# Kernel optimization log

Measured on AMD Instinct MI355X. Metric: run time of the kernel, lower is better.

## Reference

```python
import jax, jax.numpy as jnp
import numpy as np

Vx, Vy, B, N, C, H, M_VIEWS = 8, 8, 4, 196, 768, 12, 4
DH = C // H
SCALE = DH ** -0.5
HID = 4 * C


def _layer_norm(x, w, b, eps=1e-5):
    mu = jnp.mean(x, axis=-1, keepdims=True)
    var = jnp.mean((x - mu) ** 2, axis=-1, keepdims=True)
    return (x - mu) / jnp.sqrt(var + eps) * w + b


def setup_inputs() -> dict:
    key = jax.random.key(0)
    ks = jax.random.split(key, 32)
    s = 0.02
    inp = {
        "xs": jax.random.normal(ks[0], (Vx, B, N, C), jnp.float32),
        "ys": jax.random.normal(ks[1], (Vy, B, N, C), jnp.float32),
        "xposes": jax.random.randint(ks[2], (Vx, B, N, 2), 0, N),
        "yposes": jax.random.randint(ks[3], (Vy, B, N, 2), 0, N),
        "rel_ids": jax.random.randint(ks[4], (Vx * M_VIEWS,), 0, Vy),
        "M": M_VIEWS,
        # self-attention params (qkv_bias=False, proj has bias)
        "qkv_w": jax.random.normal(ks[5], (3 * C, C), jnp.float32) * s,
        "attn_proj_w": jax.random.normal(ks[6], (C, C), jnp.float32) * s,
        "attn_proj_b": jnp.zeros((C,), jnp.float32),
        # cross-attention params
        "q_w": jax.random.normal(ks[7], (C, C), jnp.float32) * s,
        "k_w": jax.random.normal(ks[8], (C, C), jnp.float32) * s,
        "v_w": jax.random.normal(ks[9], (C, C), jnp.float32) * s,
        "cross_proj_w": jax.random.normal(ks[10], (C, C), jnp.float32) * s,
        "cross_proj_b": jnp.zeros((C,), jnp.float32),
        # MLP
        "fc1_w": jax.random.normal(ks[11], (HID, C), jnp.float32) * s,
        "fc1_b": jnp.zeros((HID,), jnp.float32),
        "fc2_w": jax.random.normal(ks[12], (C, HID), jnp.float32) * s,
        "fc2_b": jnp.zeros((C,), jnp.float32),
        # layer norms
        "ln1_w": jnp.ones((C,), jnp.float32), "ln1_b": jnp.zeros((C,), jnp.float32),
        "ln2_w": jnp.ones((C,), jnp.float32), "ln2_b": jnp.zeros((C,), jnp.float32),
        "ln3_w": jnp.ones((C,), jnp.float32), "ln3_b": jnp.zeros((C,), jnp.float32),
        "lny_w": jnp.ones((C,), jnp.float32), "lny_b": jnp.zeros((C,), jnp.float32),
    }
    return inp


def _forward(xs, ys, rel_ids, M,
             qkv_w, attn_proj_w, attn_proj_b,
             q_w, k_w, v_w, cross_proj_w, cross_proj_b,
             fc1_w, fc1_b, fc2_w, fc2_b,
             ln1_w, ln1_b, ln2_w, ln2_b, ln3_w, ln3_b, lny_w, lny_b):
    vx, b, nx, c = xs.shape
    vy, _, ny, _ = ys.shape
    x = xs.reshape(vx * b, nx, c)

    # ---- self-attention over each target view (rope=None) ----
    h = _layer_norm(x, ln1_w, ln1_b)
    qkv = (h @ qkv_w.T).reshape(vx * b, nx, 3, H, DH)
    q = jnp.transpose(qkv[:, :, 0], (0, 2, 1, 3))  # (VB,H,N,dh)
    k = jnp.transpose(qkv[:, :, 1], (0, 2, 1, 3))
    v = jnp.transpose(qkv[:, :, 2], (0, 2, 1, 3))
    attn = jax.nn.softmax(jnp.einsum('bhnd,bhkd->bhnk', q, k) * SCALE, axis=-1)
    o = jnp.einsum('bhnk,bhkd->bnhd', attn, v).reshape(vx * b, nx, c)
    x = x + (o @ attn_proj_w.T + attn_proj_b)

    # ---- batched multi-view cross-attention ----
    xn = _layer_norm(x.reshape(vx, b, nx, c), ln2_w, ln2_b)
    yn = _layer_norm(ys, lny_w, lny_b)
    qs = (xn @ q_w.T).reshape(vx, b, nx, H, DH)
    ks = (yn @ k_w.T).reshape(vy, b, ny, H, DH)
    vs = (yn @ v_w.T).reshape(vy, b, ny, H, DH)
    ks_r = ks[rel_ids].reshape(vx, M, b, ny, H, DH)  # index_select + group
    vs_r = vs[rel_ids].reshape(vx, M, b, ny, H, DH)
    # q is broadcast across the M group dim (no materialized expand)
    scores = jnp.einsum('vbnhd,vmbkhd->vmbhnk', qs, ks_r) * SCALE
    a = jax.nn.softmax(scores, axis=-1)
    o = jnp.einsum('vmbhnk,vmbkhd->vmbnhd', a, vs_r).reshape(vx, M, b, nx, c)
    o = o @ cross_proj_w.T + cross_proj_b  # (Vx,M,B,Nx,C)
    merged = jnp.max(o, axis=1).reshape(vx * b, nx, c)  # max-merge over M
    x = x + merged

    # ---- MLP ----
    h = _layer_norm(x, ln3_w, ln3_b)
    x = x + (jax.nn.gelu(h @ fc1_w.T + fc1_b, approximate=False) @ fc2_w.T + fc2_b)
    return x.reshape(vx, b, nx, c)


def reference(xs, ys, xposes, yposes, rel_ids, M,
              qkv_w, attn_proj_w, attn_proj_b,
              q_w, k_w, v_w, cross_proj_w, cross_proj_b,
              fc1_w, fc1_b, fc2_w, fc2_b,
              ln1_w, ln1_b, ln2_w, ln2_b, ln3_w, ln3_b, lny_w, lny_b):
    # xposes/yposes unused because rope=None in this configuration
    return _forward(xs, ys, rel_ids, M,
                    qkv_w, attn_proj_w, attn_proj_b,
                    q_w, k_w, v_w, cross_proj_w, cross_proj_b,
                    fc1_w, fc1_b, fc2_w, fc2_b,
                    ln1_w, ln1_b, ln2_w, ln2_b, ln3_w, ln3_b, lny_w, lny_b)
```

## Files before the change

kernel.cpp:

```cpp
#include <hip/hip_runtime.h>
#include <hip/hip_bf16.h>
#include <stdint.h>
#include <math.h>

#define H_ 12
#define NQ 196
#define CD 768
#define HIDD 3072
#define VX 8
#define VY 8
#define BB 4
#define MV 4
#define VBB 32
#define ROWS 6272
#define CROSS_ROWS 25088
#define SCALE_LOG2E 0.180336880260608f

typedef __attribute__((ext_vector_type(8))) short short8;
typedef __attribute__((ext_vector_type(4))) float f32x4;
typedef __attribute__((ext_vector_type(4))) unsigned short u16x4;
typedef unsigned short u16;

#define AS1 __attribute__((address_space(1)))
#define AS3 __attribute__((address_space(3)))

__device__ __forceinline__ float bf2f(u16 u){
  union { unsigned int i; float f; } v; v.i = ((unsigned int)u) << 16; return v.f;
}
__device__ __forceinline__ u16 f2bf(float f){
  union { unsigned int i; float f; } v; v.f = f;
  return (u16)((v.i + 0x7fff + ((v.i >> 16) & 1)) >> 16);
}
__device__ __forceinline__ unsigned int f2u(float f){
  union { unsigned int i; float f; } v; v.f = f; return v.i;
}

struct CastSegs {
  const float* src[8];
  u16* dst[8];
  int cum[9];
};
__global__ __launch_bounds__(256) void k_cast_all(CastSegs segs){
  int i = blockIdx.x * 256 + threadIdx.x;
  if (i >= segs.cum[8]) return;
  int s = 0;
  #pragma unroll
  for (int k = 1; k < 8; k++) s += (i >= segs.cum[k]);
  const int off = i - segs.cum[s];
  segs.dst[s][off] = f2bf(segs.src[s][off]);
}

__device__ __forceinline__ void ln_row(const float* __restrict__ x,
    const float* __restrict__ w, const float* __restrict__ b,
    u16* __restrict__ out, int row, int tid){
  const float* xr = x + (size_t)row * CD;
  float v0 = xr[tid], v1 = xr[tid + 256], v2 = xr[tid + 512];
  float s  = v0 + v1 + v2;
  float s2 = v0*v0 + v1*v1 + v2*v2;
  __shared__ float red[8];
  const int lane = tid & 63, wid = tid >> 6;
  #pragma unroll
  for (int o = 32; o; o >>= 1){ s += __shfl_down(s, o); s2 += __shfl_down(s2, o); }
  if (lane == 0){ red[wid] = s; red[wid + 4] = s2; }
  __syncthreads();
  if (tid == 0){
    red[0] = red[0] + red[1] + red[2] + red[3];
    red[4] = red[4] + red[5] + red[6] + red[7];
  }
  __syncthreads();
  const float mu   = red[0] * (1.f/768.f);
  const float var  = red[4] * (1.f/768.f) - mu*mu;
  const float rstd = rsqrtf(var + 1e-5f);
  u16* orow = out + (size_t)row * CD;
  orow[tid]       = f2bf((v0 - mu)*rstd*w[tid]       + b[tid]);
  orow[tid + 256] = f2bf((v1 - mu)*rstd*w[tid + 256] + b[tid + 256]);
  orow[tid + 512] = f2bf((v2 - mu)*rstd*w[tid + 512] + b[tid + 512]);
}

__global__ __launch_bounds__(256) void k_ln_bf16(const float* __restrict__ x,
    const float* __restrict__ w, const float* __restrict__ b, u16* __restrict__ out){
  ln_row(x, w, b, out, blockIdx.x, threadIdx.x);
}

__global__ __launch_bounds__(256) void k_ln_bf16x2(
    const float* __restrict__ x0, const float* __restrict__ w0,
    const float* __restrict__ b0, u16* __restrict__ o0,
    const float* __restrict__ x1, const float* __restrict__ w1,
    const float* __restrict__ b1, u16* __restrict__ o1){
  const int bid = blockIdx.x;
  if (bid < ROWS) ln_row(x0, w0, b0, o0, bid, threadIdx.x);
  else            ln_row(x1, w1, b1, o1, bid - ROWS, threadIdx.x);
}

__global__ __launch_bounds__(256) void k_mmln(const u16* __restrict__ op,
    float* __restrict__ x, const float* __restrict__ w, const float* __restrict__ b,
    u16* __restrict__ out){
  const int row = blockIdx.x, tid = threadIdx.x;
  const int n = row % NQ, vb = row / NQ;
  const int vx = vb >> 2, bb = vb & 3;
  const size_t r0 = ((size_t)(vx * MV) * BB + bb) * NQ + n;
  const size_t ms = (size_t)BB * NQ;
  float* xr = x + (size_t)row * CD;
  float v[3], s = 0.f, s2 = 0.f;
  #pragma unroll
  for (int j = 0; j < 3; j++){
    const int col = tid + j*256;
    float mx =        bf2f(op[(r0       ) * CD + col]);
    mx = fmaxf(mx,    bf2f(op[(r0 +   ms) * CD + col]));
    mx = fmaxf(mx,    bf2f(op[(r0 + 2*ms) * CD + col]));
    mx = fmaxf(mx,    bf2f(op[(r0 + 3*ms) * CD + col]));
    const float val = xr[col] + mx;
    xr[col] = val;
    v[j] = val;
    s += val; s2 += val*val;
  }
  __shared__ float red[8];
  const int lane = tid & 63, wid = tid >> 6;
  #pragma unroll
  for (int o = 32; o; o >>= 1){ s += __shfl_down(s, o); s2 += __shfl_down(s2, o); }
  if (lane == 0){ red[wid] = s; red[wid + 4] = s2; }
  __syncthreads();
  if (tid == 0){
    red[0] = red[0] + red[1] + red[2] + red[3];
    red[4] = red[4] + red[5] + red[6] + red[7];
  }
  __syncthreads();
  const float mu   = red[0] * (1.f/768.f);
  const float var  = red[4] * (1.f/768.f) - mu*mu;
  const float rstd = rsqrtf(var + 1e-5f);
  u16* orow = out + (size_t)row * CD;
  #pragma unroll
  for (int j = 0; j < 3; j++){
    const int col = tid + j*256;
    orow[col] = f2bf((v[j] - mu)*rstd*w[col] + b[col]);
  }
}

template<int EPI, int TM, int DB>
__global__ __launch_bounds__(256) void k_gemm_bt(
    const u16* __restrict__ A, const u16* __restrict__ B,
    float* __restrict__ Cf, u16* __restrict__ Cb,
    const float* __restrict__ bias, const float* __restrict__ resid,
    int M, int N, int K){
  __shared__ u16 As[(DB + 1) * TM * 64];
  __shared__ u16 Bs[(DB + 1) * 128 * 64];
  const int tid  = threadIdx.x;
  const int lane = tid & 63;
  const int wave = tid >> 6;
  const int wr = wave >> 1, wc = wave & 1;

  const int gx = gridDim.x;
  const int nwg = gx * gridDim.y;
  const int orig = blockIdx.y * gx + blockIdx.x;
  const int q8 = nwg >> 3, r8 = nwg & 7;
  const int xcd = orig & 7, bse = orig >> 3;
  const int wg = (xcd < r8 ? xcd * (q8 + 1) : r8 * (q8 + 1) + (xcd - r8) * q8) + bse;
  const int m0 = (wg / gx) * TM, n0 = (wg % gx) * 128;

  f32x4 acc[TM/32][4];
  #pragma unroll
  for (int i = 0; i < TM/32; i++)
    #pragma unroll
    for (int j = 0; j < 4; j++) acc[i][j] = (f32x4){0.f, 0.f, 0.f, 0.f};

  const int lrow = lane >> 3;
  const int lcol = ((lane & 7) ^ lrow) * 8;
  const u16* arow = A + (size_t)(m0 + wave*(TM/4) + lrow) * K + lcol;
  const u16* brow = B + (size_t)(n0 + wave*32 + lrow) * K + lcol;

  auto STG = [&](int nb, int k0){
    #pragma unroll
    for (int i = 0; i < TM/32; i++)
      __builtin_amdgcn_global_load_lds(
        (const AS1 void*)(arow + (size_t)i*8*K + k0),
        (AS3 void*)(As + nb*TM*64 + (wave*(TM/4) + i*8)*64), 16, 0, 0);
    #pragma unroll
    for (int i = 0; i < 4; i++)
      __builtin_amdgcn_global_load_lds(
        (const AS1 void*)(brow + (size_t)i*8*K + k0),
        (AS3 void*)(Bs + nb*128*64 + (wave*32 + i*8)*64), 16, 0, 0);
  };

  auto COMPUTE = [&](int nb){
    const u16* ab = As + nb*TM*64 + (wr*(TM/2) + (lane & 15))*64;
    const u16* bb = Bs + nb*128*64 + (wc*64 + (lane & 15))*64;
    const int r7 = lane & 7;
    #pragma unroll
    for (int kk = 0; kk < 2; kk++){
      const int sl = (((lane >> 4) + 4*kk) ^ r7) * 8;
      short8 af[TM/32], bfr[4];
      #pragma unroll
      for (int f = 0; f < TM/32; f++) af[f] = *(const short8*)(ab + f*1024 + sl);
      #pragma unroll
      for (int f = 0; f < 4; f++)     bfr[f] = *(const short8*)(bb + f*1024 + sl);
      #pragma unroll
      for (int i = 0; i < TM/32; i++)
        #pragma unroll
        for (int j = 0; j < 4; j++)
          acc[i][j] = __builtin_amdgcn_mfma_f32_16x16x32_bf16(af[i], bfr[j], acc[i][j], 0, 0, 0);
    }
  };

  if (DB){
    const int NT = K >> 6;
    STG(0, 0);
    __syncthreads();
    for (int it = 0; it < NT; ++it){
      const int cb = it & 1;
      if (it + 1 < NT) STG(cb ^ 1, (it + 1) * 64);
      COMPUTE(cb);
      __syncthreads();
    }
  } else {
    for (int k0 = 0; k0 < K; k0 += 64){
      STG(0, k0);
      __syncthreads();
      COMPUTE(0);
      __syncthreads();
    }
  }

  #pragma unroll
  for (int i = 0; i < TM/32; i++){
    const int rb = m0 + wr*(TM/2) + i*16 + (lane >> 4)*4;
    #pragma unroll
    for (int j = 0; j < 4; j++){
      const int col = n0 + wc*64 + j*16 + (lane & 15);
      #pragma unroll
      for (int r = 0; r < 4; r++){
        const size_t idx = (size_t)(rb + r) * N + col;
        const float v = acc[i][j][r];
        if (EPI == 0){
          Cb[idx] = f2bf(v);
        } else if (EPI == 1){
          Cf[idx] = v + bias[col] + resid[idx];
        } else if (EPI == 2){
          Cf[idx] = v + bias[col];
        } else if (EPI == 3){
          float g = v + bias[col];
          g = 0.5f * g * (1.f + erff(g * 0.70710678118654752f));
          Cb[idx] = f2bf(g);
        } else {
          Cb[idx] = f2bf(v + bias[col]);
        }
      }
    }
  }
}

template<int MODE>
__global__ __launch_bounds__(256) void k_attn_mfma(
    const u16* __restrict__ Qb, const u16* __restrict__ Kb, const u16* __restrict__ Vb,
    u16* __restrict__ Ob, const int* __restrict__ rel_ids){
  __shared__ u16 Kl[2][2048];
  __shared__ u16 Vl[2][2048];

  size_t qbase, kbase, vbase, obase;
  int qstr, kstr;
  if (MODE == 0){
    const int vb = blockIdx.x / H_, h = blockIdx.x % H_;
    qbase = (size_t)vb * NQ * 2304 + h * 64; qstr = 2304;
    kbase = qbase + 768; vbase = qbase + 1536; kstr = 2304;
    obase = (size_t)vb * NQ * CD + h * 64;
  } else {
    const int h = blockIdx.x % H_; int t = blockIdx.x / H_;
    const int b = t % BB; t /= BB;
    const int m = t % MV; const int vx = t / MV;
    const int rel = rel_ids[vx * MV + m];
    qbase = ((size_t)(vx * BB + b) * NQ) * CD + h * 64; qstr = CD;
    kbase = ((size_t)(rel * BB + b) * NQ) * 1536 + h * 64; kstr = 1536;
    vbase = kbase + 768;
    obase = ((size_t)((vx * MV + m) * BB + b) * NQ) * CD + h * 64;
  }

  const int tid  = threadIdx.x;
  const int lane = tid & 63;
  const int wave = tid >> 6;
  const int lq   = lane & 15;
  const int g    = lane >> 4;

  short8 qfrag[4][2];
  #pragma unroll
  for (int qf = 0; qf < 4; qf++){
    int qrow = wave*64 + qf*16 + lq; if (qrow > 195) qrow = 195;
    const u16* qp = Qb + qbase + (size_t)qrow * qstr + g*8;
    qfrag[qf][0] = *(const short8*)(qp);
    qfrag[qf][1] = *(const short8*)(qp + 32);
  }

  f32x4 oacc[4][4];
  #pragma unroll
  for (int i = 0; i < 4; i++)
    #pragma unroll
    for (int j = 0; j < 4; j++) oacc[i][j] = (f32x4){0.f,0.f,0.f,0.f};
  float l_[4] = {0.f, 0.f, 0.f, 0.f};

  const int skey  = tid >> 3;
  const int sslot = (tid & 7) ^ (skey & 7);
  const int vkey = lane >> 1;
  const int vdh  = wave*16 + (lane & 1)*8;

  auto STAGE = [&](int nb, int t0n){
    int kg = t0n + skey; if (kg > 195) kg = 195;
    __builtin_amdgcn_global_load_lds(
        (const AS1 void*)(Kb + kbase + (size_t)kg*kstr + sslot*8),
        (AS3 void*)(&Kl[nb][wave*512]), 16, 0, 0);
    int vg = t0n + vkey; if (vg > 195) vg = 195;
    __builtin_amdgcn_global_load_lds(
        (const AS1 void*)(Vb + vbase + (size_t)vg*kstr + vdh),
        (AS3 void*)(&Vl[nb][wave*512]), 16, 0, 0);
  };

  union U8 { unsigned u[4]; short8 s; };

  STAGE(0, 0);
  __syncthreads();

  for (int t = 0; t < 7; t++){
    const int cb = t & 1;
    const int t0 = t * 32;
    if (t < 6) STAGE(cb ^ 1, t0 + 32);

    f32x4 sacc[4][2];
    #pragma unroll
    for (int qf = 0; qf < 4; qf++)
      #pragma unroll
      for (int kf = 0; kf < 2; kf++) sacc[qf][kf] = (f32x4){0.f,0.f,0.f,0.f};
    __builtin_amdgcn_s_setprio(1);
    #pragma unroll
    for (int kf = 0; kf < 2; kf++){
      const int key = kf*16 + lq;
      #pragma unroll
      for (int ks = 0; ks < 2; ks++){
        short8 kfrag = *(const short8*)(&Kl[cb][key*64 + (((ks<<2) + g) ^ (key & 7))*8]);
        #pragma unroll
        for (int qf = 0; qf < 4; qf++)
          if (wave*64 + qf*16 < NQ)
            sacc[qf][kf] = __builtin_amdgcn_mfma_f32_16x16x32_bf16(kfrag, qfrag[qf][ks], sacc[qf][kf], 0, 0, 0);
      }
    }
    __builtin_amdgcn_s_setprio(0);

    const AS3 u16* vp = (const AS3 u16*)(&Vl[cb][0]) + (size_t)lane*4;
    uint2 tr0a, tr0b, tr1a, tr1b, tr2a, tr2b, tr3a, tr3b;
    asm volatile("ds_read_b64_tr_b16 %0, %1 offset:0"    : "=&v"(tr0a) : "v"(vp));
    asm volatile("ds_read_b64_tr_b16 %0, %1 offset:512"  : "=&v"(tr0b) : "v"(vp));
    asm volatile("ds_read_b64_tr_b16 %0, %1 offset:1024" : "=&v"(tr1a) : "v"(vp));
    asm volatile("ds_read_b64_tr_b16 %0, %1 offset:1536" : "=&v"(tr1b) : "v"(vp));
    asm volatile("ds_read_b64_tr_b16 %0, %1 offset:2048" : "=&v"(tr2a) : "v"(vp));
    asm volatile("ds_read_b64_tr_b16 %0, %1 offset:2560" : "=&v"(tr2b) : "v"(vp));
    asm volatile("ds_read_b64_tr_b16 %0, %1 offset:3072" : "=&v"(tr3a) : "v"(vp));
    asm volatile("ds_read_b64_tr_b16 %0, %1 offset:3584" : "=&v"(tr3b) : "v"(vp));

    short8 vfrag[4];
    #pragma unroll
    for (int qf = 0; qf < 4; qf++){
      if (wave*64 + qf*16 >= NQ) continue;
      float p[8], ps = 0.f;
      #pragma unroll
      for (int kf = 0; kf < 2; kf++)
        #pragma unroll
        for (int r = 0; r < 4; r++){
          const int key = t0 + kf*16 + g*4 + r;
          const float e = exp2f(sacc[qf][kf][r] * SCALE_LOG2E);
          p[kf*4 + r] = (key < 196) ? e : 0.f;
          ps += p[kf*4 + r];
        }
      ps += __shfl_xor(ps, 16);
      ps += __shfl_xor(ps, 32);
      l_[qf] += ps;
      U8 pk;
      pk.u[0] = (f2u(p[0]) >> 16) | (f2u(p[1]) & 0xffff0000u);
      pk.u[1] = (f2u(p[2]) >> 16) | (f2u(p[3]) & 0xffff0000u);
      pk.u[2] = (f2u(p[4]) >> 16) | (f2u(p[5]) & 0xffff0000u);
      pk.u[3] = (f2u(p[6]) >> 16) | (f2u(p[7]) & 0xffff0000u);

      if (qf == 0){
        asm volatile("s_waitcnt lgkmcnt(0)" ::: "memory");
        __builtin_amdgcn_sched_barrier(0);
        U8 v0; v0.u[0]=tr0a.x; v0.u[1]=tr0a.y; v0.u[2]=tr0b.x; v0.u[3]=tr0b.y; vfrag[0]=v0.s;
        U8 v1; v1.u[0]=tr1a.x; v1.u[1]=tr1a.y; v1.u[2]=tr1b.x; v1.u[3]=tr1b.y; vfrag[1]=v1.s;
        U8 v2; v2.u[0]=tr2a.x; v2.u[1]=tr2a.y; v2.u[2]=tr2b.x; v2.u[3]=tr2b.y; vfrag[2]=v2.s;
        U8 v3; v3.u[0]=tr3a.x; v3.u[1]=tr3a.y; v3.u[2]=tr3b.x; v3.u[3]=tr3b.y; vfrag[3]=v3.s;
      }
      __builtin_amdgcn_s_setprio(1);
      #pragma unroll
      for (int dhf = 0; dhf < 4; dhf++)
        oacc[qf][dhf] = __builtin_amdgcn_mfma_f32_16x16x32_bf16(vfrag[dhf], pk.s, oacc[qf][dhf], 0, 0, 0);
      __builtin_amdgcn_s_setprio(0);
    }
    __syncthreads();
  }

  #pragma unroll
  for (int qf = 0; qf < 4; qf++){
    const int qrow = wave*64 + qf*16 + lq;
    if (qrow < 196){
      const float inv = 1.f / l_[qf];
      u16* orow = Ob + obase + (size_t)qrow * CD;
      #pragma unroll
      for (int dhf = 0; dhf < 4; dhf++){
        uint2 pk;
        pk.x = (unsigned)f2bf(oacc[qf][dhf][0]*inv) | ((unsigned)f2bf(oacc[qf][dhf][1]*inv) << 16);
        pk.y = (unsigned)f2bf(oacc[qf][dhf][2]*inv) | ((unsigned)f2bf(oacc[qf][dhf][3]*inv) << 16);
        *(uint2*)(orow + dhf*16 + g*4) = pk;
      }
    }
  }
}

extern "C" void kernel_launch(void* const* d_in, const int* in_sizes, int n_in,
                              void* d_out, int out_size, void* d_ws, size_t ws_size,
                              hipStream_t stream){
  const float* xs           = (const float*)d_in[0];
  const float* ys           = (const float*)d_in[1];
  const int*   rel_ids      = (const int*)  d_in[4];
  const float* qkv_w        = (const float*)d_in[6];
  const float* attn_proj_w  = (const float*)d_in[7];
  const float* attn_proj_b  = (const float*)d_in[8];
  const float* q_w          = (const float*)d_in[9];
  const float* k_w          = (const float*)d_in[10];
  const float* v_w          = (const float*)d_in[11];
  const float* cross_proj_w = (const float*)d_in[12];
  const float* cross_proj_b = (const float*)d_in[13];
  const float* fc1_w        = (const float*)d_in[14];
  const float* fc1_b        = (const float*)d_in[15];
  const float* fc2_w        = (const float*)d_in[16];
  const float* fc2_b        = (const float*)d_in[17];
  const float* ln1_w        = (const float*)d_in[18];
  const float* ln1_b        = (const float*)d_in[19];
  const float* ln2_w        = (const float*)d_in[20];
  const float* ln2_b        = (const float*)d_in[21];
  const float* ln3_w        = (const float*)d_in[22];
  const float* ln3_b        = (const float*)d_in[23];
  const float* lny_w        = (const float*)d_in[24];
  const float* lny_b        = (const float*)d_in[25];
  float* out = (float*)d_out;

  char* ws = (char*)d_ws;
  size_t off = 0;
  auto alloc = [&](size_t bytes) -> char* {
    char* p = ws + off; off += (bytes + 255) & ~(size_t)255; return p;
  };
  u16* wb_qkv   = (u16*)alloc((size_t)2304*768*2);
  u16* wb_aproj = (u16*)alloc((size_t)768*768*2);
  u16* wb_q     = (u16*)alloc((size_t)768*768*2);
  u16* wb_kv    = (u16*)alloc((size_t)1536*768*2);
  u16* wb_cproj = (u16*)alloc((size_t)768*768*2);
  u16* wb_fc1   = (u16*)alloc((size_t)3072*768*2);
  u16* wb_fc2   = (u16*)alloc((size_t)768*3072*2);
  float* x_ws   = (float*)alloc((size_t)ROWS*CD*4);
  u16* hbuf     = (u16*)alloc((size_t)ROWS*CD*2);
  u16* ynbuf    = (u16*)alloc((size_t)ROWS*CD*2);
  u16* o_self   = (u16*)alloc((size_t)ROWS*CD*2);
  u16* qs       = (u16*)alloc((size_t)ROWS*CD*2);
  u16* kvs      = (u16*)alloc((size_t)ROWS*1536*2);
  u16* o_cross  = (u16*)alloc((size_t)CROSS_ROWS*CD*2);
  char* un = alloc((size_t)CROSS_ROWS*CD*2);
  u16* qkvbuf = (u16*)un;
  u16* oproj  = (u16*)un;
  u16* mid    = (u16*)un;

  CastSegs segs;
  const float* srcs[8] = {qkv_w, attn_proj_w, q_w, k_w, v_w, cross_proj_w, fc1_w, fc2_w};
  u16* dsts[8] = {wb_qkv, wb_aproj, wb_q, wb_kv, wb_kv + 768*768, wb_cproj, wb_fc1, wb_fc2};
  int lens[8]  = {2304*768, 768*768, 768*768, 768*768, 768*768, 768*768, 3072*768, 3072*768};
  segs.cum[0] = 0;
  for (int i = 0; i < 8; i++){ segs.src[i] = srcs[i]; segs.dst[i] = dsts[i];
                               segs.cum[i+1] = segs.cum[i] + lens[i]; }
  k_cast_all<<<(segs.cum[8] + 255) / 256, 256, 0, stream>>>(segs);

  k_ln_bf16<<<ROWS, 256, 0, stream>>>(xs, ln1_w, ln1_b, hbuf);
  k_gemm_bt<0,128,0><<<dim3(2304/128, ROWS/128), 256, 0, stream>>>(
      hbuf, wb_qkv, nullptr, qkvbuf, nullptr, nullptr, ROWS, 2304, 768);
  k_attn_mfma<0><<<VBB * H_, 256, 0, stream>>>(qkvbuf, qkvbuf, qkvbuf, o_self, rel_ids);
  k_gemm_bt<1,64,1><<<dim3(768/128, ROWS/64), 256, 0, stream>>>(
      o_self, wb_aproj, x_ws, nullptr, attn_proj_b, xs, ROWS, 768, 768);

  k_ln_bf16x2<<<2*ROWS, 256, 0, stream>>>(x_ws, ln2_w, ln2_b, hbuf,
                                          ys, lny_w, lny_b, ynbuf);
  k_gemm_bt<0,64,1><<<dim3(768/128, ROWS/64), 256, 0, stream>>>(
      hbuf, wb_q, nullptr, qs, nullptr, nullptr, ROWS, 768, 768);
  k_gemm_bt<0,128,0><<<dim3(1536/128, ROWS/128), 256, 0, stream>>>(
      ynbuf, wb_kv, nullptr, kvs, nullptr, nullptr, ROWS, 1536, 768);
  k_attn_mfma<1><<<VX * MV * BB * H_, 256, 0, stream>>>(qs, kvs, kvs, o_cross, rel_ids);
  k_gemm_bt<4,128,0><<<dim3(768/128, CROSS_ROWS/128), 256, 0, stream>>>(
      o_cross, wb_cproj, nullptr, oproj, cross_proj_b, nullptr, CROSS_ROWS, 768, 768);
  k_mmln<<<ROWS, 256, 0, stream>>>(oproj, x_ws, ln3_w, ln3_b, hbuf);

  k_gemm_bt<3,128,0><<<dim3(HIDD/128, ROWS/128), 256, 0, stream>>>(
      hbuf, wb_fc1, nullptr, mid, fc1_b, nullptr, ROWS, HIDD, 768);
  k_gemm_bt<1,64,1><<<dim3(768/128, ROWS/64), 256, 0, stream>>>(
      mid, wb_fc2, out, nullptr, fc2_b, x_ws, ROWS, 768, HIDD);
}
```

Measured before the change: 380.9 us.

## Fold softmax scale into Q GEMM epilogue and compute row sums via MFMA

Adds a GEMM epilogue that multiplies the Q columns by scale*log2e before the bf16 store, so attention exponentiates raw scores without a per-element multiply. The softmax denominator is now accumulated with an extra MFMA against a vector of bf16 ones, which replaces the per-element sums and cross-lane shuffles. Key-boundary masking runs only on the last tile, and the row-validity guards around the MFMAs are dropped so the unrolled loops are uniform. In exchange, Q is rounded to bf16 after scaling, the denominator is summed from bf16-rounded probabilities, and padded query rows do redundant MFMA work.

```diff
diff --git a/kernel.cpp b/kernel.cpp
--- a/kernel.cpp
+++ b/kernel.cpp
@@ -240,8 +240,10 @@
           float g = v + bias[col];
           g = 0.5f * g * (1.f + erff(g * 0.70710678118654752f));
           Cb[idx] = f2bf(g);
+        } else if (EPI == 4){
+          Cb[idx] = f2bf(v + bias[col]);
         } else {
-          Cb[idx] = f2bf(v + bias[col]);
+          Cb[idx] = f2bf(col < 768 ? v * SCALE_LOG2E : v);
         }
       }
     }
@@ -288,12 +290,19 @@
     qfrag[qf][1] = *(const short8*)(qp + 32);
   }
 
+  union U8 { unsigned u[4]; short8 s; };
+
   f32x4 oacc[4][4];
   #pragma unroll
   for (int i = 0; i < 4; i++)
     #pragma unroll
     for (int j = 0; j < 4; j++) oacc[i][j] = (f32x4){0.f,0.f,0.f,0.f};
-  float l_[4] = {0.f, 0.f, 0.f, 0.f};
+  f32x4 lacc[4];
+  #pragma unroll
+  for (int i = 0; i < 4; i++) lacc[i] = (f32x4){0.f,0.f,0.f,0.f};
+  U8 ones;
+  #pragma unroll
+  for (int i = 0; i < 4; i++) ones.u[i] = 0x3F803F80u;
 
   const int skey  = tid >> 3;
   const int sslot = (tid & 7) ^ (skey & 7);
@@ -311,8 +320,6 @@
         (AS3 void*)(&Vl[nb][wave*512]), 16, 0, 0);
   };
 
-  union U8 { unsigned u[4]; short8 s; };
-
   STAGE(0, 0);
   __syncthreads();
 
@@ -335,8 +342,7 @@
         short8 kfrag = *(const short8*)(&Kl[cb][key*64 + (((ks<<2) + g) ^ (key & 7))*8]);
         #pragma unroll
         for (int qf = 0; qf < 4; qf++)
-          if (wave*64 + qf*16 < NQ)
-            sacc[qf][kf] = __builtin_amdgcn_mfma_f32_16x16x32_bf16(kfrag, qfrag[qf][ks], sacc[qf][kf], 0, 0, 0);
+          sacc[qf][kf] = __builtin_amdgcn_mfma_f32_16x16x32_bf16(kfrag, qfrag[qf][ks], sacc[qf][kf], 0, 0, 0);
       }
     }
     __builtin_amdgcn_s_setprio(0);
@@ -355,20 +361,19 @@
     short8 vfrag[4];
     #pragma unroll
     for (int qf = 0; qf < 4; qf++){
-      if (wave*64 + qf*16 >= NQ) continue;
-      float p[8], ps = 0.f;
+      float p[8];
       #pragma unroll
       for (int kf = 0; kf < 2; kf++)
         #pragma unroll
-        for (int r = 0; r < 4; r++){
-          const int key = t0 + kf*16 + g*4 + r;
-          const float e = exp2f(sacc[qf][kf][r] * SCALE_LOG2E);
-          p[kf*4 + r] = (key < 196) ? e : 0.f;
-          ps += p[kf*4 + r];
-        }
-      ps += __shfl_xor(ps, 16);
-      ps += __shfl_xor(ps, 32);
-      l_[qf] += ps;
+        for (int r = 0; r < 4; r++)
+          p[kf*4 + r] = exp2f(sacc[qf][kf][r]);
+      if (t == 6){
+        #pragma unroll
+        for (int kf = 0; kf < 2; kf++)
+          #pragma unroll
+          for (int r = 0; r < 4; r++)
+            if (192 + kf*16 + g*4 + r >= NQ) p[kf*4 + r] = 0.f;
+      }
       U8 pk;
       pk.u[0] = (f2u(p[0]) >> 16) | (f2u(p[1]) & 0xffff0000u);
       pk.u[1] = (f2u(p[2]) >> 16) | (f2u(p[3]) & 0xffff0000u);
@@ -387,6 +392,7 @@
       #pragma unroll
       for (int dhf = 0; dhf < 4; dhf++)
         oacc[qf][dhf] = __builtin_amdgcn_mfma_f32_16x16x32_bf16(vfrag[dhf], pk.s, oacc[qf][dhf], 0, 0, 0);
+      lacc[qf] = __builtin_amdgcn_mfma_f32_16x16x32_bf16(ones.s, pk.s, lacc[qf], 0, 0, 0);
       __builtin_amdgcn_s_setprio(0);
     }
     __syncthreads();
@@ -396,7 +402,7 @@
   for (int qf = 0; qf < 4; qf++){
     const int qrow = wave*64 + qf*16 + lq;
     if (qrow < 196){
-      const float inv = 1.f / l_[qf];
+      const float inv = 1.f / lacc[qf][0];
       u16* orow = Ob + obase + (size_t)qrow * CD;
       #pragma unroll
       for (int dhf = 0; dhf < 4; dhf++){
@@ -471,7 +477,7 @@
   k_cast_all<<<(segs.cum[8] + 255) / 256, 256, 0, stream>>>(segs);
 
   k_ln_bf16<<<ROWS, 256, 0, stream>>>(xs, ln1_w, ln1_b, hbuf);
-  k_gemm_bt<0,128,0><<<dim3(2304/128, ROWS/128), 256, 0, stream>>>(
+  k_gemm_bt<5,128,0><<<dim3(2304/128, ROWS/128), 256, 0, stream>>>(
       hbuf, wb_qkv, nullptr, qkvbuf, nullptr, nullptr, ROWS, 2304, 768);
   k_attn_mfma<0><<<VBB * H_, 256, 0, stream>>>(qkvbuf, qkvbuf, qkvbuf, o_self, rel_ids);
   k_gemm_bt<1,64,1><<<dim3(768/128, ROWS/64), 256, 0, stream>>>(
@@ -479,7 +485,7 @@
 
   k_ln_bf16x2<<<2*ROWS, 256, 0, stream>>>(x_ws, ln2_w, ln2_b, hbuf,
                                           ys, lny_w, lny_b, ynbuf);
-  k_gemm_bt<0,64,1><<<dim3(768/128, ROWS/64), 256, 0, stream>>>(
+  k_gemm_bt<5,64,1><<<dim3(768/128, ROWS/64), 256, 0, stream>>>(
       hbuf, wb_q, nullptr, qs, nullptr, nullptr, ROWS, 768, 768);
   k_gemm_bt<0,128,0><<<dim3(1536/128, ROWS/128), 256, 0, stream>>>(
       ynbuf, wb_kv, nullptr, kvs, nullptr, nullptr, ROWS, 1536, 768);
```

Result: no change. 374.7 us (-1.6%).
